# Kernel optimization log

Hardware: AMD Instinct MI355X
Metric: run time of the kernel (lower is better)

## Reference

```python
import jax, jax.numpy as jnp
import numpy as np

INPUT_SIZE = 2048
HIDDEN_SIZE = 2048
BATCH = 4096


def setup_inputs() -> dict:
    key = jax.random.key(0)
    ks = jax.random.split(key, 12)
    std = 1.0 / HIDDEN_SIZE ** 0.5
    def u(k, shape):
        return jax.random.uniform(k, shape, jnp.float32, -std, std)
    inp = {
        "x": jax.random.normal(ks[0], (BATCH, INPUT_SIZE), jnp.float32),
        "h": jax.random.normal(ks[1], (BATCH, HIDDEN_SIZE), jnp.float32),
        "c": jax.random.normal(ks[2], (BATCH, HIDDEN_SIZE), jnp.float32),
        "weight_ii": u(ks[3], (HIDDEN_SIZE, INPUT_SIZE)),
        "weight_if": u(ks[4], (HIDDEN_SIZE, INPUT_SIZE)),
        "weight_ig": u(ks[5], (HIDDEN_SIZE, INPUT_SIZE)),
        "weight_io": u(ks[6], (HIDDEN_SIZE, INPUT_SIZE)),
        "weight_hi": u(ks[7], (HIDDEN_SIZE, HIDDEN_SIZE)),
        "weight_hf": u(ks[8], (HIDDEN_SIZE, HIDDEN_SIZE)),
        "weight_hg": u(ks[9], (HIDDEN_SIZE, HIDDEN_SIZE)),
        "weight_ho": u(ks[10], (HIDDEN_SIZE, HIDDEN_SIZE)),
        "bias_i": u(ks[11], (HIDDEN_SIZE,)),
        "bias_f": u(jax.random.fold_in(key, 100), (HIDDEN_SIZE,)),
        "bias_g": u(jax.random.fold_in(key, 101), (HIDDEN_SIZE,)),
        "bias_o": u(jax.random.fold_in(key, 102), (HIDDEN_SIZE,)),
    }
    return inp


def reference(x, h, c, weight_ii, weight_if, weight_ig, weight_io,
              weight_hi, weight_hf, weight_hg, weight_ho,
              bias_i, bias_f, bias_g, bias_o):
    # Fuse the 4 input projections and 4 hidden projections into 2 GEMMs
    # (same math as 8 separate matmuls in the original module).
    W_x = jnp.concatenate([weight_ii, weight_if, weight_ig, weight_io], axis=0)  # [4H, I]
    W_h = jnp.concatenate([weight_hi, weight_hf, weight_hg, weight_ho], axis=0)  # [4H, H]
    b = jnp.concatenate([bias_i, bias_f, bias_g, bias_o], axis=0)                # [4H]
    gates = x @ W_x.T + h @ W_h.T + b                                            # [B, 4H]
    gi, gf, gg, go = jnp.split(gates, 4, axis=1)
    i = jax.nn.sigmoid(gi)
    f = jax.nn.sigmoid(gf)
    g = jnp.tanh(gg)
    o = jax.nn.sigmoid(go)
    c_new = f * c + i * g
    h_new = o * jnp.tanh(c_new)
    return (h_new, c_new)
```

## Files before the change

kernel.cpp:

```cpp
#include <hip/hip_runtime.h>
#include <cstdint>
#include <cstddef>

#define BATCH 4096
#define HID   2048
#define NT    64

typedef __attribute__((ext_vector_type(8))) short bf16x8;
typedef __attribute__((ext_vector_type(4))) float f32x4;

__device__ __forceinline__ unsigned short f2bf(float f) {
  union { float f; unsigned u; } a; a.f = f;
  unsigned u = a.u;
  return (unsigned short)((u + 0x7FFFu + ((u >> 16) & 1u)) >> 16);
}

__device__ __forceinline__ void gload_lds16(const void* g, void* l) {
  __builtin_amdgcn_global_load_lds((const __attribute__((address_space(1))) void*)g,
                                   (__attribute__((address_space(3))) void*)l, 16, 0, 0);
}

#define SCHED0() __builtin_amdgcn_sched_barrier(0)
#define SBAR()  do { SCHED0(); __builtin_amdgcn_s_barrier(); SCHED0(); } while (0)
#define WAITV(N) do { SCHED0(); asm volatile("s_waitcnt vmcnt(" #N ")" ::: "memory"); SCHED0(); } while (0)
#define WAITL(N) do { SCHED0(); asm volatile("s_waitcnt lgkmcnt(" #N ")" ::: "memory"); SCHED0(); } while (0)
#define DSR_(dst, adr, S) asm volatile("ds_read_b128 %0, %1 offset:" S : "=v"(dst) : "v"(adr))
#define DSR(dst, adr, IMM) DSR_(dst, adr, #IMM)

#define READ_CLUSTER(AADR, BADR) do { \
  DSR(a1[0], (AADR), 0); DSR(a1[1], (AADR), 1024); DSR(a1[2], (AADR), 2048); DSR(a1[3], (AADR), 3072); \
  DSR(bf_[0], (BADR), 0); DSR(bf_[1], (BADR), 1024); DSR(bf_[2], (BADR), 2048); DSR(bf_[3], (BADR), 3072); \
  DSR(a2[0], (AADR), 4096); DSR(a2[1], (AADR), 5120); DSR(a2[2], (AADR), 6144); DSR(a2[3], (AADR), 7168); \
} while (0)

#define MFMA_HALF(AF, OFS) do { \
  _Pragma("unroll") \
  for (int m_ = 0; m_ < 4; m_++) { \
    _Pragma("unroll") \
    for (int n_ = 0; n_ < 4; n_++) \
      acc[(OFS) + m_][n_] = __builtin_amdgcn_mfma_f32_16x16x32_bf16(AF[m_], bf_[n_], acc[(OFS) + m_][n_], 0, 0, 0); \
  } \
} while (0)

__global__ __launch_bounds__(256) void convert_kernel(
    const float* __restrict__ x, const float* __restrict__ h,
    const float* __restrict__ wii, const float* __restrict__ wif,
    const float* __restrict__ wig, const float* __restrict__ wio,
    const float* __restrict__ whi, const float* __restrict__ whf,
    const float* __restrict__ whg, const float* __restrict__ who,
    unsigned short* __restrict__ Abf, unsigned short* __restrict__ Wbf) {
  int seg = blockIdx.y;
  const float* src;
  unsigned short* dst;
  int ofs;
  size_t rofs;
  if (seg < 4) {
    src = (seg < 2) ? x : h;
    dst = Abf;
    ofs = (seg < 2) ? 0 : 2048;
    rofs = (seg & 1) ? 2048 : 0;
    src += rofs * 2048;
  } else {
    int g = (seg - 4) & 3;
    dst = Wbf + (size_t)g * 2048 * 4096;
    ofs = (seg >= 8) ? 2048 : 0;
    rofs = 0;
    switch (seg) {
      case 4: src = wii; break; case 5: src = wif; break;
      case 6: src = wig; break; case 7: src = wio; break;
      case 8: src = whi; break; case 9: src = whf; break;
      case 10: src = whg; break; default: src = who; break;
    }
  }
  size_t idx = (size_t)blockIdx.x * 256 + threadIdx.x;
  size_t e = idx * 4;
  int n = (int)(e >> 11);
  int k = (int)(e & 2047);
  float4 v = *(const float4*)(src + e);
  ushort4 o;
  o.x = f2bf(v.x); o.y = f2bf(v.y); o.z = f2bf(v.z); o.w = f2bf(v.w);
  *(ushort4*)(dst + (rofs + (size_t)n) * 4096 + ofs + k) = o;
}

__global__ __launch_bounds__(512, 2) void lstm_gemm8(
    const unsigned short* __restrict__ Abf, const unsigned short* __restrict__ Wbf,
    const float* __restrict__ c_in,
    const float* __restrict__ bias_i, const float* __restrict__ bias_f,
    const float* __restrict__ bias_g, const float* __restrict__ bias_o,
    float* __restrict__ out) {
  __shared__ unsigned short lds[2][4][256 * 32];

  int tid = threadIdx.x;
  int lane = tid & 63;
  int wid = tid >> 6;
  int wr = wid >> 2;
  int wc = wid & 3;
  int lrow = lane & 15;
  int qh = lane >> 4;

  int bid = blockIdx.x;
  int xcd = bid & 7;
  int t7 = bid >> 3;
  int mt = t7 & 15;
  int bn = xcd * 4 + (t7 >> 4);
  int m0 = mt * 256;

  int r0 = tid >> 2, cc0 = tid & 3;
  int ccs0 = cc0 ^ ((r0 >> 1) & 3);
  const unsigned short* pA = Abf + (size_t)(m0 + r0) * 4096 + ccs0 * 8;
  int g0 = (r0 >> 4) & 3;
  int jw = bn * 64 + ((r0 >> 6) & 3) * 16 + (r0 & 15);
  const unsigned short* pB = Wbf + ((size_t)g0 * 2048 + jw) * 4096 + ccs0 * 8;

  char* L0 = (char*)&lds[0][0][0];
  char* dA = L0 + tid * 16;
  unsigned ldsOff = (unsigned)(size_t)(__attribute__((address_space(3))) char*)L0;

  int arow0 = wr * 128 + lrow;
  int brow0 = wc * 64 + lrow;
  unsigned qsA = ((unsigned)(qh ^ ((arow0 >> 1) & 3))) << 4;
  unsigned qsB = ((unsigned)(qh ^ ((brow0 >> 1) & 3))) << 4;
  unsigned aB0 = ldsOff + (unsigned)arow0 * 64 + qsA;
  unsigned bB0 = ldsOff + 16384u + (unsigned)brow0 * 64 + qsB;

  f32x4 acc[8][4];
  #pragma unroll
  for (int a = 0; a < 8; a++)
    #pragma unroll
    for (int b = 0; b < 4; b++) acc[a][b] = (f32x4){0.f, 0.f, 0.f, 0.f};

  gload_lds16(pA, dA);
  gload_lds16(pA + 128 * 4096, dA + 8192);
  gload_lds16(pB, dA + 16384);
  gload_lds16(pB + 32 * 4096, dA + 16384 + 8192);
  gload_lds16(pA + 32, dA + 32768);
  gload_lds16(pA + 128 * 4096 + 32, dA + 32768 + 8192);
  gload_lds16(pB + 32, dA + 49152);
  gload_lds16(pB + 32 * 4096 + 32, dA + 49152 + 8192);
  WAITV(4);
  SBAR();

  bf16x8 a1[4], a2[4], bf_[4];

  for (int t = 0; t < NT - 1; ++t) {
    int b = t & 1;
    unsigned bufo = b ? 65536u : 0u;
    char* nD = dA + (b ? 0 : 65536);
    unsigned aAdr = aB0 + bufo;
    unsigned bAdr = bB0 + bufo;
    int k1 = (t + 1) * 64;

    READ_CLUSTER(aAdr, bAdr);
    gload_lds16(pA + k1, nD);
    gload_lds16(pA + 128 * 4096 + k1, nD + 8192);
    WAITL(4);
    __builtin_amdgcn_s_setprio(1);
    MFMA_HALF(a1, 0);
    __builtin_amdgcn_s_setprio(0);
    gload_lds16(pB + k1, nD + 16384);
    gload_lds16(pB + 32 * 4096 + k1, nD + 16384 + 8192);
    WAITL(0);
    __builtin_amdgcn_s_setprio(1);
    MFMA_HALF(a2, 4);
    __builtin_amdgcn_s_setprio(0);
    WAITV(4);
    SBAR();

    READ_CLUSTER(aAdr + 32768u, bAdr + 32768u);
    gload_lds16(pA + k1 + 32, nD + 32768);
    gload_lds16(pA + 128 * 4096 + k1 + 32, nD + 32768 + 8192);
    WAITL(4);
    __builtin_amdgcn_s_setprio(1);
    MFMA_HALF(a1, 0);
    __builtin_amdgcn_s_setprio(0);
    gload_lds16(pB + k1 + 32, nD + 49152);
    gload_lds16(pB + 32 * 4096 + k1 + 32, nD + 49152 + 8192);
    WAITL(0);
    __builtin_amdgcn_s_setprio(1);
    MFMA_HALF(a2, 4);
    __builtin_amdgcn_s_setprio(0);
    WAITV(4);
    SBAR();
  }

  {
    unsigned aAdr = aB0 + 65536u;
    unsigned bAdr = bB0 + 65536u;
    READ_CLUSTER(aAdr, bAdr);
    WAITL(4);
    MFMA_HALF(a1, 0);
    WAITL(0);
    MFMA_HALF(a2, 4);
    WAITV(0);
    SBAR();
    READ_CLUSTER(aAdr + 32768u, bAdr + 32768u);
    WAITL(4);
    MFMA_HALF(a1, 0);
    WAITL(0);
    MFMA_HALF(a2, 4);
  }

  int j = bn * 64 + wc * 16 + lrow;
  float bi = bias_i[j], bff = bias_f[j], bgg = bias_g[j], bo = bias_o[j];
  int rbase = m0 + wr * 128 + qh * 4;
  #pragma unroll
  for (int mf = 0; mf < 8; mf++) {
    #pragma unroll
    for (int qq = 0; qq < 4; qq++) {
      int m = rbase + mf * 16 + qq;
      size_t off = (size_t)m * HID + j;
      float gi = acc[mf][0][qq] + bi;
      float gf = acc[mf][1][qq] + bff;
      float gg = acc[mf][2][qq] + bgg;
      float go = acc[mf][3][qq] + bo;
      float iv = 1.f / (1.f + __expf(-gi));
      float fv = 1.f / (1.f + __expf(-gf));
      float gv = tanhf(gg);
      float ov = 1.f / (1.f + __expf(-go));
      float cn = fv * c_in[off] + iv * gv;
      float hn = ov * tanhf(cn);
      out[off] = hn;
      out[(size_t)BATCH * HID + off] = cn;
    }
  }
}

__global__ __launch_bounds__(256) void lstm_gemm_fb(
    const float* __restrict__ x, const float* __restrict__ h,
    const float* __restrict__ wii, const float* __restrict__ wif,
    const float* __restrict__ wig, const float* __restrict__ wio,
    const float* __restrict__ whi, const float* __restrict__ whf,
    const float* __restrict__ whg, const float* __restrict__ who,
    const float* __restrict__ c_in,
    const float* __restrict__ bias_i, const float* __restrict__ bias_f,
    const float* __restrict__ bias_g, const float* __restrict__ bias_o,
    float* __restrict__ out) {
  __shared__ unsigned short Ald[128 * 64];
  __shared__ unsigned short Bld[128 * 64];
  int tid = threadIdx.x;
  int lane = tid & 63;
  int wid = tid >> 6;
  int wr = wid >> 1, wc = wid & 1;
  int bid = blockIdx.x;
  int swz = (bid & 7) * 256 + (bid >> 3);
  int mt = swz & 31;
  int ht = swz >> 5;
  int m0 = mt * 128;
  int j0 = ht * 32;
  f32x4 acc[4][4];
  #pragma unroll
  for (int a = 0; a < 4; a++)
    #pragma unroll
    for (int b = 0; b < 4; b++) acc[a][b] = (f32x4){0.f, 0.f, 0.f, 0.f};
  int lrow = lane & 15;
  int lsw = lrow & 7;
  int qbase = lane >> 4;
  for (int kt = 0; kt < 64; kt++) {
    int k0 = kt * 64;
    const float* Asrc = (k0 < 2048) ? x : h;
    int ka = k0 & 2047;
    #pragma unroll
    for (int i = 0; i < 4; i++) {
      int c = i * 256 + tid;
      int r = c >> 3, cc = c & 7;
      int ccs = cc ^ (r & 7);
      const float* s = Asrc + (size_t)(m0 + r) * 2048 + ka + ccs * 8;
      float4 v0 = *(const float4*)s;
      float4 v1 = *(const float4*)(s + 4);
      bf16x8 pk;
      pk[0] = (short)f2bf(v0.x); pk[1] = (short)f2bf(v0.y);
      pk[2] = (short)f2bf(v0.z); pk[3] = (short)f2bf(v0.w);
      pk[4] = (short)f2bf(v1.x); pk[5] = (short)f2bf(v1.y);
      pk[6] = (short)f2bf(v1.z); pk[7] = (short)f2bf(v1.w);
      *(bf16x8*)((char*)Ald + (size_t)c * 16) = pk;
    }
    #pragma unroll
    for (int i = 0; i < 4; i++) {
      int c = i * 256 + tid;
      int rb = c >> 3, cc = c & 7;
      int ccs = cc ^ (rb & 7);
      int g = rb >> 5, jj = rb & 31;
      const float* Bsrc;
      if (k0 < 2048) Bsrc = (g == 0) ? wii : (g == 1) ? wif : (g == 2) ? wig : wio;
      else           Bsrc = (g == 0) ? whi : (g == 1) ? whf : (g == 2) ? whg : who;
      const float* s = Bsrc + (size_t)(j0 + jj) * 2048 + ka + ccs * 8;
      float4 v0 = *(const float4*)s;
      float4 v1 = *(const float4*)(s + 4);
      bf16x8 pk;
      pk[0] = (short)f2bf(v0.x); pk[1] = (short)f2bf(v0.y);
      pk[2] = (short)f2bf(v0.z); pk[3] = (short)f2bf(v0.w);
      pk[4] = (short)f2bf(v1.x); pk[5] = (short)f2bf(v1.y);
      pk[6] = (short)f2bf(v1.z); pk[7] = (short)f2bf(v1.w);
      *(bf16x8*)((char*)Bld + (size_t)c * 16) = pk;
    }
    __syncthreads();
    #pragma unroll
    for (int ks = 0; ks < 2; ks++) {
      int q = ks * 4 + qbase;
      int qs8 = (q ^ lsw) * 8;
      bf16x8 af[4], bg[4];
      #pragma unroll
      for (int mf = 0; mf < 4; mf++)
        af[mf] = *(const bf16x8*)&Ald[(wr * 64 + mf * 16 + lrow) * 64 + qs8];
      #pragma unroll
      for (int g = 0; g < 4; g++)
        bg[g] = *(const bf16x8*)&Bld[(g * 32 + wc * 16 + lrow) * 64 + qs8];
      #pragma unroll
      for (int mf = 0; mf < 4; mf++)
        #pragma unroll
        for (int g = 0; g < 4; g++)
          acc[mf][g] = __builtin_amdgcn_mfma_f32_16x16x32_bf16(af[mf], bg[g], acc[mf][g], 0, 0, 0);
    }
    __syncthreads();
  }
  int j = j0 + wc * 16 + lrow;
  float bi = bias_i[j], bff = bias_f[j], bgg = bias_g[j], bo = bias_o[j];
  int rbase = m0 + wr * 64 + (lane >> 4) * 4;
  #pragma unroll
  for (int mf = 0; mf < 4; mf++) {
    #pragma unroll
    for (int q = 0; q < 4; q++) {
      int m = rbase + mf * 16 + q;
      size_t off = (size_t)m * HID + j;
      float gi = acc[mf][0][q] + bi;
      float gf = acc[mf][1][q] + bff;
      float gg = acc[mf][2][q] + bgg;
      float go = acc[mf][3][q] + bo;
      float iv = 1.f / (1.f + __expf(-gi));
      float fv = 1.f / (1.f + __expf(-gf));
      float gv = tanhf(gg);
      float ov = 1.f / (1.f + __expf(-go));
      float cn = fv * c_in[off] + iv * gv;
      float hn = ov * tanhf(cn);
      out[off] = hn;
      out[(size_t)BATCH * HID + off] = cn;
    }
  }
}

extern "C" void kernel_launch(void* const* d_in, const int* in_sizes, int n_in,
                              void* d_out, int out_size, void* d_ws, size_t ws_size,
                              hipStream_t stream) {
  const float* x   = (const float*)d_in[0];
  const float* h   = (const float*)d_in[1];
  const float* c   = (const float*)d_in[2];
  const float* wii = (const float*)d_in[3];
  const float* wif = (const float*)d_in[4];
  const float* wig = (const float*)d_in[5];
  const float* wio = (const float*)d_in[6];
  const float* whi = (const float*)d_in[7];
  const float* whf = (const float*)d_in[8];
  const float* whg = (const float*)d_in[9];
  const float* who = (const float*)d_in[10];
  const float* bi  = (const float*)d_in[11];
  const float* bf  = (const float*)d_in[12];
  const float* bg  = (const float*)d_in[13];
  const float* bo  = (const float*)d_in[14];
  float* out = (float*)d_out;

  size_t needA = (size_t)4096 * 4096 * 2;
  size_t needW = (size_t)8192 * 4096 * 2;

  if (ws_size >= needA + needW) {
    unsigned short* Abf = (unsigned short*)d_ws;
    unsigned short* Wbf = (unsigned short*)((char*)d_ws + needA);
    convert_kernel<<<dim3(4096, 12), 256, 0, stream>>>(
        x, h, wii, wif, wig, wio, whi, whf, whg, who, Abf, Wbf);
    lstm_gemm8<<<512, 512, 0, stream>>>(Abf, Wbf, c, bi, bf, bg, bo, out);
  } else {
    lstm_gemm_fb<<<2048, 256, 0, stream>>>(
        x, h, wii, wif, wig, wio, whi, whf, whg, who,
        c, bi, bf, bg, bo, out);
  }
}
```

Baseline: 317.3 us.

## Restructure GEMM main loop into four-slot LDS pipeline with register double-buffering

Replaces the two-buffer, two-half-step loop with four 32-wide K slots in LDS. Global loads are issued three slots ahead, and the A-lo and B fragments for the next slot are prefetched into alternating register sets (a1A/bfA and a1B/bfB) while the current MFMAs run. This aims to hide both global-load latency and LDS-read latency behind MFMA work, and to need one barrier per 32-wide slot. The cost is more VGPRs for the duplicated fragment registers and more complex waitcnt accounting, which could cut occupancy or introduce ordering hazards.

After: 315.7 us (median of 2 runs). No clear change (-0.5%).

```diff
diff --git a/kernel.cpp b/kernel.cpp
--- a/kernel.cpp
+++ b/kernel.cpp
@@ -24,22 +24,41 @@
 #define SBAR()  do { SCHED0(); __builtin_amdgcn_s_barrier(); SCHED0(); } while (0)
 #define WAITV(N) do { SCHED0(); asm volatile("s_waitcnt vmcnt(" #N ")" ::: "memory"); SCHED0(); } while (0)
 #define WAITL(N) do { SCHED0(); asm volatile("s_waitcnt lgkmcnt(" #N ")" ::: "memory"); SCHED0(); } while (0)
-#define DSR_(dst, adr, S) asm volatile("ds_read_b128 %0, %1 offset:" S : "=v"(dst) : "v"(adr))
-#define DSR(dst, adr, IMM) DSR_(dst, adr, #IMM)
-
-#define READ_CLUSTER(AADR, BADR) do { \
-  DSR(a1[0], (AADR), 0); DSR(a1[1], (AADR), 1024); DSR(a1[2], (AADR), 2048); DSR(a1[3], (AADR), 3072); \
-  DSR(bf_[0], (BADR), 0); DSR(bf_[1], (BADR), 1024); DSR(bf_[2], (BADR), 2048); DSR(bf_[3], (BADR), 3072); \
-  DSR(a2[0], (AADR), 4096); DSR(a2[1], (AADR), 5120); DSR(a2[2], (AADR), 6144); DSR(a2[3], (AADR), 7168); \
-} while (0)
-
-#define MFMA_HALF(AF, OFS) do { \
-  _Pragma("unroll") \
-  for (int m_ = 0; m_ < 4; m_++) { \
-    _Pragma("unroll") \
+#define DSR(dst, adr, IMM) asm volatile("ds_read_b128 %0, %1 offset:" #IMM : "=v"(dst) : "v"(adr))
+
+#define RD_A2_LO(ADR) do { DSR(a2[0],ADR,4096); DSR(a2[1],ADR,5120); DSR(a2[2],ADR,6144); DSR(a2[3],ADR,7168); } while (0)
+#define RD_A2_HI(ADR) do { DSR(a2[0],ADR,36864); DSR(a2[1],ADR,37888); DSR(a2[2],ADR,38912); DSR(a2[3],ADR,39936); } while (0)
+#define RD_N_LO(AADR,BADR,A1,BF) do { \
+  DSR(A1[0],AADR,0); DSR(A1[1],AADR,1024); DSR(A1[2],AADR,2048); DSR(A1[3],AADR,3072); \
+  DSR(BF[0],BADR,0); DSR(BF[1],BADR,1024); DSR(BF[2],BADR,2048); DSR(BF[3],BADR,3072); } while (0)
+#define RD_N_HI(AADR,BADR,A1,BF) do { \
+  DSR(A1[0],AADR,32768); DSR(A1[1],AADR,33792); DSR(A1[2],AADR,34816); DSR(A1[3],AADR,35840); \
+  DSR(BF[0],BADR,32768); DSR(BF[1],BADR,33792); DSR(BF[2],BADR,34816); DSR(BF[3],BADR,35840); } while (0)
+
+#define MFMA_LO(A1, BF) do { _Pragma("unroll") \
+  for (int m_ = 0; m_ < 4; m_++) { _Pragma("unroll") \
     for (int n_ = 0; n_ < 4; n_++) \
-      acc[(OFS) + m_][n_] = __builtin_amdgcn_mfma_f32_16x16x32_bf16(AF[m_], bf_[n_], acc[(OFS) + m_][n_], 0, 0, 0); \
-  } \
+      acc[m_][n_] = __builtin_amdgcn_mfma_f32_16x16x32_bf16(A1[m_], BF[n_], acc[m_][n_], 0, 0, 0); } } while (0)
+#define MFMA_HI(BF) do { _Pragma("unroll") \
+  for (int m_ = 0; m_ < 4; m_++) { _Pragma("unroll") \
+    for (int n_ = 0; n_ < 4; n_++) \
+      acc[4+m_][n_] = __builtin_amdgcn_mfma_f32_16x16x32_bf16(a2[m_], BF[n_], acc[4+m_][n_], 0, 0, 0); } } while (0)
+
+#define STAGE_G(KOFF, DOF) do { \
+  gload_lds16(pA + (KOFF), dA + (DOF)); \
+  gload_lds16(pA + 128*4096 + (KOFF), dA + (DOF) + 8192); \
+  gload_lds16(pB + (KOFF), dA + (DOF) + 16384); \
+  gload_lds16(pB + 32*4096 + (KOFF), dA + (DOF) + 16384 + 8192); } while (0)
+
+#define SLOT(TOPV, RDA2CALL, RDNCALL, STAGECALL, MA1, MBF) do { \
+  TOPV; SBAR(); WAITL(0); \
+  RDA2CALL; \
+  RDNCALL; \
+  STAGECALL; \
+  SCHED0(); \
+  __builtin_amdgcn_s_setprio(1); MFMA_LO(MA1, MBF); __builtin_amdgcn_s_setprio(0); \
+  WAITL(8); \
+  __builtin_amdgcn_s_setprio(1); MFMA_HI(MBF); __builtin_amdgcn_s_setprio(0); \
 } while (0)
 
 __global__ __launch_bounds__(256) void convert_kernel(
@@ -120,8 +139,10 @@
   int brow0 = wc * 64 + lrow;
   unsigned qsA = ((unsigned)(qh ^ ((arow0 >> 1) & 3))) << 4;
   unsigned qsB = ((unsigned)(qh ^ ((brow0 >> 1) & 3))) << 4;
-  unsigned aB0 = ldsOff + (unsigned)arow0 * 64 + qsA;
-  unsigned bB0 = ldsOff + 16384u + (unsigned)brow0 * 64 + qsB;
+  unsigned a0 = ldsOff + (unsigned)arow0 * 64 + qsA;
+  unsigned b0 = ldsOff + 16384u + (unsigned)brow0 * 64 + qsB;
+  unsigned a1v = a0 + 65536u;
+  unsigned b1v = b0 + 65536u;
 
   f32x4 acc[8][4];
   #pragma unroll
@@ -129,76 +150,32 @@
     #pragma unroll
     for (int b = 0; b < 4; b++) acc[a][b] = (f32x4){0.f, 0.f, 0.f, 0.f};
 
-  gload_lds16(pA, dA);
-  gload_lds16(pA + 128 * 4096, dA + 8192);
-  gload_lds16(pB, dA + 16384);
-  gload_lds16(pB + 32 * 4096, dA + 16384 + 8192);
-  gload_lds16(pA + 32, dA + 32768);
-  gload_lds16(pA + 128 * 4096 + 32, dA + 32768 + 8192);
-  gload_lds16(pB + 32, dA + 49152);
-  gload_lds16(pB + 32 * 4096 + 32, dA + 49152 + 8192);
-  WAITV(4);
+  bf16x8 a1A[4], bfA[4], a1B[4], bfB[4], a2[4];
+
+  STAGE_G(0, 0);
+  STAGE_G(32, 32768);
+  STAGE_G(64, 65536);
+  WAITV(8);
   SBAR();
-
-  bf16x8 a1[4], a2[4], bf_[4];
-
-  for (int t = 0; t < NT - 1; ++t) {
-    int b = t & 1;
-    unsigned bufo = b ? 65536u : 0u;
-    char* nD = dA + (b ? 0 : 65536);
-    unsigned aAdr = aB0 + bufo;
-    unsigned bAdr = bB0 + bufo;
-    int k1 = (t + 1) * 64;
-
-    READ_CLUSTER(aAdr, bAdr);
-    gload_lds16(pA + k1, nD);
-    gload_lds16(pA + 128 * 4096 + k1, nD + 8192);
-    WAITL(4);
-    __builtin_amdgcn_s_setprio(1);
-    MFMA_HALF(a1, 0);
-    __builtin_amdgcn_s_setprio(0);
-    gload_lds16(pB + k1, nD + 16384);
-    gload_lds16(pB + 32 * 4096 + k1, nD + 16384 + 8192);
-    WAITL(0);
-    __builtin_amdgcn_s_setprio(1);
-    MFMA_HALF(a2, 4);
-    __builtin_amdgcn_s_setprio(0);
-    WAITV(4);
-    SBAR();
-
-    READ_CLUSTER(aAdr + 32768u, bAdr + 32768u);
-    gload_lds16(pA + k1 + 32, nD + 32768);
-    gload_lds16(pA + 128 * 4096 + k1 + 32, nD + 32768 + 8192);
-    WAITL(4);
-    __builtin_amdgcn_s_setprio(1);
-    MFMA_HALF(a1, 0);
-    __builtin_amdgcn_s_setprio(0);
-    gload_lds16(pB + k1 + 32, nD + 49152);
-    gload_lds16(pB + 32 * 4096 + k1 + 32, nD + 49152 + 8192);
-    WAITL(0);
-    __builtin_amdgcn_s_setprio(1);
-    MFMA_HALF(a2, 4);
-    __builtin_amdgcn_s_setprio(0);
-    WAITV(4);
-    SBAR();
-  }
-
-  {
-    unsigned aAdr = aB0 + 65536u;
-    unsigned bAdr = bB0 + 65536u;
-    READ_CLUSTER(aAdr, bAdr);
-    WAITL(4);
-    MFMA_HALF(a1, 0);
-    WAITL(0);
-    MFMA_HALF(a2, 4);
-    WAITV(0);
-    SBAR();
-    READ_CLUSTER(aAdr + 32768u, bAdr + 32768u);
-    WAITL(4);
-    MFMA_HALF(a1, 0);
-    WAITL(0);
-    MFMA_HALF(a2, 4);
-  }
+  RD_N_LO(a0, b0, a1A, bfA);
+
+  for (int i = 0; i < 31; ++i) {
+    int kb = i * 128;
+    SLOT(WAITV(4), RD_A2_LO(a0), RD_N_HI(a0, b0, a1B, bfB), STAGE_G(kb + 96, 98304), a1A, bfA);
+    SLOT(WAITV(4), RD_A2_HI(a0), RD_N_LO(a1v, b1v, a1A, bfA), STAGE_G(kb + 128, 0), a1B, bfB);
+    SLOT(WAITV(4), RD_A2_LO(a1v), RD_N_HI(a1v, b1v, a1B, bfB), STAGE_G(kb + 160, 32768), a1A, bfA);
+    SLOT(WAITV(4), RD_A2_HI(a1v), RD_N_LO(a0, b0, a1A, bfA), STAGE_G(kb + 192, 65536), a1B, bfB);
+  }
+
+  SLOT(WAITV(4), RD_A2_LO(a0), RD_N_HI(a0, b0, a1B, bfB), STAGE_G(4064, 98304), a1A, bfA);
+  SLOT(WAITV(4), RD_A2_HI(a0), RD_N_LO(a1v, b1v, a1A, bfA), (void)0, a1B, bfB);
+  SLOT(WAITV(0), RD_A2_LO(a1v), RD_N_HI(a1v, b1v, a1B, bfB), (void)0, a1A, bfA);
+  WAITL(0);
+  RD_A2_HI(a1v);
+  SCHED0();
+  __builtin_amdgcn_s_setprio(1); MFMA_LO(a1B, bfB); __builtin_amdgcn_s_setprio(0);
+  WAITL(0);
+  __builtin_amdgcn_s_setprio(1); MFMA_HI(bfB); __builtin_amdgcn_s_setprio(0);
 
   int j = bn * 64 + wc * 16 + lrow;
   float bi = bias_i[j], bff = bias_f[j], bgg = bias_g[j], bo = bias_o[j];
```
